# Performance work log

Hardware: AMD Instinct MI355X
Metric: run time of the kernel (lower is better)

## Reference

```python
import jax, jax.numpy as jnp
import numpy as np

B, D, H = 4096, 1024, 1024  # batch, input_size, hidden_size


def setup_inputs() -> dict:
    key = jax.random.key(0)
    ks = jax.random.split(key, 7)
    stdv = 1.0 / np.sqrt(H)
    u = lambda k, shape: jax.random.uniform(k, shape, jnp.float32, -stdv, stdv)
    return {
        "x": jax.random.normal(ks[0], (B, D), jnp.float32),
        "h0": jax.random.normal(ks[1], (1, B, H), jnp.float32),
        "c0": jax.random.normal(ks[2], (1, B, H), jnp.float32),
        "w_ih": u(ks[3], (4 * H, D)),
        "w_hh": u(ks[4], (4 * H, H)),
        "b_ih": u(ks[5], (4 * H,)),
        "b_hh": u(ks[6], (4 * H,)),
    }


def lstm_cell(x, h, c, w_ih, w_hh, b_ih, b_hh):
    # gates: [B, 4H] = x @ w_ih^T + b_ih + h @ w_hh^T + b_hh
    gates = x @ w_ih.T + h @ w_hh.T + (b_ih + b_hh)
    i, f, g, o = jnp.split(gates, 4, axis=1)
    c_new = jax.nn.sigmoid(f) * c + jax.nn.sigmoid(i) * jnp.tanh(g)
    h_new = jax.nn.sigmoid(o) * jnp.tanh(c_new)
    return h_new, c_new


def reference(x, h0, c0, w_ih, w_hh, b_ih, b_hh):
    # num_layers = 1 (the only well-formed config of the original module)
    h, c = lstm_cell(x, h0[0], c0[0], w_ih, w_hh, b_ih, b_hh)
    return h, c
```

## Files before the change

kernel.cpp:

```cpp
#include <hip/hip_runtime.h>
#include <hip/hip_bf16.h>

#define TB 4096
#define TD 1024
#define TH 1024
#define TK 2048
#define NT 64
#define BUF_SZ 32768
#define B_OFF 16384

typedef _Float16 f16;
typedef _Float16 f16x8 __attribute__((ext_vector_type(8)));
typedef _Float16 f16x4 __attribute__((ext_vector_type(4)));
typedef float f32x4 __attribute__((ext_vector_type(4)));

__device__ __forceinline__ void gload16(const f16* g, const char* l) {
  __builtin_amdgcn_global_load_lds(
      (const __attribute__((address_space(1))) void*)g,
      (__attribute__((address_space(3))) void*)l, 16, 0, 0);
}

__global__ void __launch_bounds__(256) k_convert(
    const float* __restrict__ x, const float* __restrict__ h0,
    const float* __restrict__ w_ih, const float* __restrict__ w_hh,
    f16* __restrict__ Uh, f16* __restrict__ Wh) {
  int t = blockIdx.x * 256 + threadIdx.x;
  const int perMat = (TB * TK) / 4;
  const bool isW = t >= perMat;
  int tt = isW ? t - perMat : t;
  size_t e0 = (size_t)tt * 4;
  int row = (int)(e0 >> 11);
  int k = (int)(e0 & (TK - 1));
  const float* src;
  if (!isW)
    src = (k < TD) ? (x + (size_t)row * TD + k) : (h0 + (size_t)row * TH + (k - TD));
  else
    src = (k < TD) ? (w_ih + (size_t)row * TD + k) : (w_hh + (size_t)row * TH + (k - TD));
  float4 v = *(const float4*)src;
  f16x4 o;
  o[0] = (f16)v.x; o[1] = (f16)v.y; o[2] = (f16)v.z; o[3] = (f16)v.w;
  *(f16x4*)((isW ? Wh : Uh) + e0) = o;
}

__global__ void __launch_bounds__(512, 2) k_lstm(
    const f16* __restrict__ Uh, const f16* __restrict__ Wh,
    const float* __restrict__ b_ih, const float* __restrict__ b_hh,
    const float* __restrict__ c0, float* __restrict__ h_out,
    float* __restrict__ c_out) {
  extern __shared__ char lds[];
  const int tid = threadIdx.x;
  const int l = tid & 63;
  const int w = tid >> 6;
  const int wm = w >> 2;
  const int wc = w & 3;

  int bid = blockIdx.x;
  int swz = (bid & 7) * 32 + (bid >> 3);
  const int bm = swz >> 4;
  const int bn = swz & 15;
  const int rowBase = bm * 256;
  const int hcBase = bn * 64;

  const int g = (l & 3) ^ ((l >> 3) & 3);
  const int rl = l >> 2;
  const int cA0 = w, cA1 = 8 + w;
  const f16* aP0 = Uh + (size_t)(rowBase + cA0 * 16 + rl) * TK + g * 8;
  const f16* aP1 = Uh + (size_t)(rowBase + cA1 * 16 + rl) * TK + g * 8;
  const f16* bP0 = Wh + (size_t)((cA0 & 3) * 1024 + hcBase + rl + (cA0 >> 2) * 16) * TK + g * 8;
  const f16* bP1 = Wh + (size_t)((cA1 & 3) * 1024 + hcBase + rl + (cA1 >> 2) * 16) * TK + g * 8;

  const int fr = l & 15;
  const int fq = l >> 4;
  const int slot = ((fq ^ ((fr >> 1) & 3)) << 4);
  const int aAddr = (wm * 128 + fr) * 64 + slot;
  const int bAddr = B_OFF + (wc * 64 + fr) * 64 + slot;

  f32x4 acc[8][4] = {};

  gload16(aP0, lds + 0 * BUF_SZ + cA0 * 1024);
  gload16(aP1, lds + 0 * BUF_SZ + cA1 * 1024);
  gload16(bP0, lds + 0 * BUF_SZ + B_OFF + cA0 * 1024);
  gload16(bP1, lds + 0 * BUF_SZ + B_OFF + cA1 * 1024);
  gload16(aP0 + 32, lds + 1 * BUF_SZ + cA0 * 1024);
  gload16(aP1 + 32, lds + 1 * BUF_SZ + cA1 * 1024);
  gload16(bP0 + 32, lds + 1 * BUF_SZ + B_OFF + cA0 * 1024);
  gload16(bP1 + 32, lds + 1 * BUF_SZ + B_OFF + cA1 * 1024);
  asm volatile("s_waitcnt vmcnt(4)" ::: "memory");
  __builtin_amdgcn_sched_barrier(0);
  __builtin_amdgcn_s_barrier();

  int offR = 0;
  int offS = 2 * BUF_SZ;
  for (int t = 0; t < NT; ++t) {
    if (t < NT - 2) {
      const int ke = (t + 2) * 32;
      gload16(aP0 + ke, lds + offS + cA0 * 1024);
      gload16(aP1 + ke, lds + offS + cA1 * 1024);
      gload16(bP0 + ke, lds + offS + B_OFF + cA0 * 1024);
      gload16(bP1 + ke, lds + offS + B_OFF + cA1 * 1024);
    }
    const char* baseA = lds + offR + aAddr;
    const char* baseB = lds + offR + bAddr;
    f16x8 af[8], bf[4];
#pragma unroll
    for (int m = 0; m < 8; ++m) af[m] = *(const f16x8*)(baseA + m * 1024);
#pragma unroll
    for (int n = 0; n < 4; ++n) bf[n] = *(const f16x8*)(baseB + n * 1024);
    __builtin_amdgcn_s_setprio(1);
#pragma unroll
    for (int m = 0; m < 8; ++m)
#pragma unroll
      for (int n = 0; n < 4; ++n)
        acc[m][n] = __builtin_amdgcn_mfma_f32_16x16x32_f16(af[m], bf[n], acc[m][n], 0, 0, 0);
    __builtin_amdgcn_s_setprio(0);
    asm volatile("s_waitcnt lgkmcnt(0)" ::: "memory");
    if (t < NT - 2)
      asm volatile("s_waitcnt vmcnt(4)" ::: "memory");
    else
      asm volatile("s_waitcnt vmcnt(0)" ::: "memory");
    __builtin_amdgcn_sched_barrier(0);
    __builtin_amdgcn_s_barrier();
    offR = (offR == 2 * BUF_SZ) ? 0 : offR + BUF_SZ;
    offS = (offS == 2 * BUF_SZ) ? 0 : offS + BUF_SZ;
  }

  const int hc = hcBase + wc * 16 + fr;
  const float bi = b_ih[hc] + b_hh[hc];
  const float bfv = b_ih[TH + hc] + b_hh[TH + hc];
  const float bg = b_ih[2 * TH + hc] + b_hh[2 * TH + hc];
  const float bo = b_ih[3 * TH + hc] + b_hh[3 * TH + hc];
#pragma unroll
  for (int m = 0; m < 8; ++m) {
#pragma unroll
    for (int r = 0; r < 4; ++r) {
      const int row = rowBase + wm * 128 + m * 16 + fq * 4 + r;
      float gi = acc[m][0][r] + bi;
      float gf = acc[m][1][r] + bfv;
      float gg = acc[m][2][r] + bg;
      float go = acc[m][3][r] + bo;
      float cprev = c0[(size_t)row * TH + hc];
      float ig = 1.0f / (1.0f + __expf(-gi));
      float fg = 1.0f / (1.0f + __expf(-gf));
      float og = 1.0f / (1.0f + __expf(-go));
      float cn = fg * cprev + ig * tanhf(gg);
      float hn = og * tanhf(cn);
      h_out[(size_t)row * TH + hc] = hn;
      c_out[(size_t)row * TH + hc] = cn;
    }
  }
}

extern "C" void kernel_launch(void* const* d_in, const int* in_sizes, int n_in,
                              void* d_out, int out_size, void* d_ws, size_t ws_size,
                              hipStream_t stream) {
  const float* x    = (const float*)d_in[0];
  const float* h0   = (const float*)d_in[1];
  const float* c0   = (const float*)d_in[2];
  const float* w_ih = (const float*)d_in[3];
  const float* w_hh = (const float*)d_in[4];
  const float* b_ih = (const float*)d_in[5];
  const float* b_hh = (const float*)d_in[6];

  float* h_out = (float*)d_out;
  float* c_out = h_out + (size_t)TB * TH;

  f16* Uh = (f16*)d_ws;
  f16* Wh = Uh + (size_t)TB * TK;

  const int convBlocks = (2 * TB * TK / 4) / 256;
  k_convert<<<convBlocks, 256, 0, stream>>>(x, h0, w_ih, w_hh, Uh, Wh);

  static_assert(3 * BUF_SZ == 98304, "lds");
  (void)hipFuncSetAttribute((const void*)k_lstm,
                            hipFuncAttributeMaxDynamicSharedMemorySize, 3 * BUF_SZ);
  k_lstm<<<256, 512, 3 * BUF_SZ, stream>>>(Uh, Wh, b_ih, b_hh, c0, h_out, c_out);
}
```

Baseline: 211.5 us.

## Deepen GEMM pipeline to four LDS stages with split half-phase barriers

Moves the LSTM GEMM main loop from a triple-buffered 96KB LDS ring to a four-stage 128KB ring. Each K-step is split into two half-phases: half the A fragments plus the B fragments, then the other half of the A fragments. The split interleaves global-to-LDS loads with the MFMA work and adds finer barriers. The goal is to hide more global latency and overlap LDS reads with MFMAs, at the cost of twice as many barriers. The 128KB of LDS per block also forces one block per CU, where launch_bounds asks for two.

```diff
diff --git a/kernel.cpp b/kernel.cpp
--- a/kernel.cpp
+++ b/kernel.cpp
@@ -5,9 +5,7 @@
 #define TD 1024
 #define TH 1024
 #define TK 2048
-#define NT 64
-#define BUF_SZ 32768
-#define B_OFF 16384
+#define NITER 16
 
 typedef _Float16 f16;
 typedef _Float16 f16x8 __attribute__((ext_vector_type(8)));
@@ -42,6 +40,35 @@
   *(f16x4*)((isW ? Wh : Uh) + e0) = o;
 }
 
+#define PH(RB, MQ, LOADB, SP0, SP1, SD, KOFF, PRED, VM)                          \
+  {                                                                              \
+    if (LOADB) {                                                                 \
+      _Pragma("unroll") for (int n = 0; n < 4; ++n)                              \
+          bf[n] = *(const f16x8*)(lds + (RB) + 16384 + bOff + n * 1024);         \
+    }                                                                            \
+    f16x8 af[4];                                                                 \
+    _Pragma("unroll") for (int m = 0; m < 4; ++m)                                \
+        af[m] = *(const f16x8*)(lds + (RB) + aOff + ((MQ) * 4 + m) * 1024);      \
+    if (PRED) {                                                                  \
+      gload16((SP0) + (KOFF), (SD));                                             \
+      gload16((SP1) + (KOFF), (SD) + 8192);                                      \
+    }                                                                            \
+    __builtin_amdgcn_s_barrier();                                                \
+    asm volatile("s_waitcnt lgkmcnt(0)" ::: "memory");                           \
+    __builtin_amdgcn_sched_barrier(0);                                           \
+    __builtin_amdgcn_s_setprio(1);                                               \
+    _Pragma("unroll") for (int m = 0; m < 4; ++m)                                \
+        _Pragma("unroll") for (int n = 0; n < 4; ++n)                            \
+            acc[(MQ) * 4 + m][n] = __builtin_amdgcn_mfma_f32_16x16x32_f16(       \
+                af[m], bf[n], acc[(MQ) * 4 + m][n], 0, 0, 0);                    \
+    __builtin_amdgcn_s_setprio(0);                                               \
+    if (VM) {                                                                    \
+      asm volatile("s_waitcnt vmcnt(8)" ::: "memory");                           \
+      __builtin_amdgcn_sched_barrier(0);                                         \
+    }                                                                            \
+    __builtin_amdgcn_s_barrier();                                                \
+  }
+
 __global__ void __launch_bounds__(512, 2) k_lstm(
     const f16* __restrict__ Uh, const f16* __restrict__ Wh,
     const float* __restrict__ b_ih, const float* __restrict__ b_hh,
@@ -61,67 +88,45 @@
   const int rowBase = bm * 256;
   const int hcBase = bn * 64;
 
+  const int rl = l >> 2;
   const int g = (l & 3) ^ ((l >> 3) & 3);
-  const int rl = l >> 2;
-  const int cA0 = w, cA1 = 8 + w;
-  const f16* aP0 = Uh + (size_t)(rowBase + cA0 * 16 + rl) * TK + g * 8;
-  const f16* aP1 = Uh + (size_t)(rowBase + cA1 * 16 + rl) * TK + g * 8;
-  const f16* bP0 = Wh + (size_t)((cA0 & 3) * 1024 + hcBase + rl + (cA0 >> 2) * 16) * TK + g * 8;
-  const f16* bP1 = Wh + (size_t)((cA1 & 3) * 1024 + hcBase + rl + (cA1 >> 2) * 16) * TK + g * 8;
+  const int c0i = w, c1i = w + 8;
+  const f16* aP0 = Uh + (size_t)(rowBase + c0i * 16 + rl) * TK + g * 8;
+  const f16* aP1 = Uh + (size_t)(rowBase + c1i * 16 + rl) * TK + g * 8;
+  const f16* bP0 = Wh + (size_t)((c0i & 3) * 1024 + hcBase + rl + (c0i >> 2) * 16) * TK + g * 8;
+  const f16* bP1 = Wh + (size_t)((c1i & 3) * 1024 + hcBase + rl + (c1i >> 2) * 16) * TK + g * 8;
+  char* sdw = lds + w * 1024;
 
   const int fr = l & 15;
   const int fq = l >> 4;
-  const int slot = ((fq ^ ((fr >> 1) & 3)) << 4);
-  const int aAddr = (wm * 128 + fr) * 64 + slot;
-  const int bAddr = B_OFF + (wc * 64 + fr) * 64 + slot;
+  const int slot = (fq ^ ((fr >> 1) & 3)) << 4;
+  const int aOff = (wm * 128 + fr) * 64 + slot;
+  const int bOff = (wc * 64 + fr) * 64 + slot;
 
   f32x4 acc[8][4] = {};
+  f16x8 bf[4];
 
-  gload16(aP0, lds + 0 * BUF_SZ + cA0 * 1024);
-  gload16(aP1, lds + 0 * BUF_SZ + cA1 * 1024);
-  gload16(bP0, lds + 0 * BUF_SZ + B_OFF + cA0 * 1024);
-  gload16(bP1, lds + 0 * BUF_SZ + B_OFF + cA1 * 1024);
-  gload16(aP0 + 32, lds + 1 * BUF_SZ + cA0 * 1024);
-  gload16(aP1 + 32, lds + 1 * BUF_SZ + cA1 * 1024);
-  gload16(bP0 + 32, lds + 1 * BUF_SZ + B_OFF + cA0 * 1024);
-  gload16(bP1 + 32, lds + 1 * BUF_SZ + B_OFF + cA1 * 1024);
-  asm volatile("s_waitcnt vmcnt(4)" ::: "memory");
+  gload16(aP0 + 0,  sdw + 0);      gload16(aP1 + 0,  sdw + 0 + 8192);
+  gload16(bP0 + 0,  sdw + 16384);  gload16(bP1 + 0,  sdw + 16384 + 8192);
+  gload16(aP0 + 32, sdw + 32768);  gload16(aP1 + 32, sdw + 32768 + 8192);
+  gload16(bP0 + 32, sdw + 49152);  gload16(bP1 + 32, sdw + 49152 + 8192);
+  gload16(aP0 + 64, sdw + 65536);  gload16(aP1 + 64, sdw + 65536 + 8192);
+  gload16(bP0 + 64, sdw + 81920);  gload16(bP1 + 64, sdw + 81920 + 8192);
+  asm volatile("s_waitcnt vmcnt(8)" ::: "memory");
   __builtin_amdgcn_sched_barrier(0);
   __builtin_amdgcn_s_barrier();
 
-  int offR = 0;
-  int offS = 2 * BUF_SZ;
-  for (int t = 0; t < NT; ++t) {
-    if (t < NT - 2) {
-      const int ke = (t + 2) * 32;
-      gload16(aP0 + ke, lds + offS + cA0 * 1024);
-      gload16(aP1 + ke, lds + offS + cA1 * 1024);
-      gload16(bP0 + ke, lds + offS + B_OFF + cA0 * 1024);
-      gload16(bP1 + ke, lds + offS + B_OFF + cA1 * 1024);
-    }
-    const char* baseA = lds + offR + aAddr;
-    const char* baseB = lds + offR + bAddr;
-    f16x8 af[8], bf[4];
-#pragma unroll
-    for (int m = 0; m < 8; ++m) af[m] = *(const f16x8*)(baseA + m * 1024);
-#pragma unroll
-    for (int n = 0; n < 4; ++n) bf[n] = *(const f16x8*)(baseB + n * 1024);
-    __builtin_amdgcn_s_setprio(1);
-#pragma unroll
-    for (int m = 0; m < 8; ++m)
-#pragma unroll
-      for (int n = 0; n < 4; ++n)
-        acc[m][n] = __builtin_amdgcn_mfma_f32_16x16x32_f16(af[m], bf[n], acc[m][n], 0, 0, 0);
-    __builtin_amdgcn_s_setprio(0);
-    asm volatile("s_waitcnt lgkmcnt(0)" ::: "memory");
-    if (t < NT - 2)
-      asm volatile("s_waitcnt vmcnt(4)" ::: "memory");
-    else
-      asm volatile("s_waitcnt vmcnt(0)" ::: "memory");
-    __builtin_amdgcn_sched_barrier(0);
-    __builtin_amdgcn_s_barrier();
-    offR = (offR == 2 * BUF_SZ) ? 0 : offR + BUF_SZ;
-    offS = (offS == 2 * BUF_SZ) ? 0 : offS + BUF_SZ;
+  for (int i = 0; i < NITER; ++i) {
+    const int kb = i * 128;
+    const bool pr = (i < NITER - 1);
+    PH(0,     0, true,  aP0, aP1, sdw + 65536 + 32768, kb + 96,  true, false)
+    PH(0,     1, false, bP0, bP1, sdw + 65536 + 49152, kb + 96,  true, true)
+    PH(32768, 0, true,  aP0, aP1, sdw + 0,             kb + 128, pr,   false)
+    PH(32768, 1, false, bP0, bP1, sdw + 16384,         kb + 128, pr,   true)
+    PH(65536, 0, true,  aP0, aP1, sdw + 32768,         kb + 160, pr,   false)
+    PH(65536, 1, false, bP0, bP1, sdw + 49152,         kb + 160, pr,   true)
+    PH(98304, 0, true,  aP0, aP1, sdw + 65536,         kb + 192, pr,   false)
+    PH(98304, 1, false, bP0, bP1, sdw + 65536 + 16384, kb + 192, pr,   true)
   }
 
   const int hc = hcBase + wc * 16 + fr;
@@ -170,8 +175,7 @@
   const int convBlocks = (2 * TB * TK / 4) / 256;
   k_convert<<<convBlocks, 256, 0, stream>>>(x, h0, w_ih, w_hh, Uh, Wh);
 
-  static_assert(3 * BUF_SZ == 98304, "lds");
   (void)hipFuncSetAttribute((const void*)k_lstm,
-                            hipFuncAttributeMaxDynamicSharedMemorySize, 3 * BUF_SZ);
-  k_lstm<<<256, 512, 3 * BUF_SZ, stream>>>(Uh, Wh, b_ih, b_hh, c0, h_out, c_out);
+                            hipFuncAttributeMaxDynamicSharedMemorySize, 131072);
+  k_lstm<<<256, 512, 131072, stream>>>(Uh, Wh, b_ih, b_hh, c0, h_out, c_out);
 }
```

After: 211.0 us. Within noise of the previous version (-0.2%).
